# Performance work log

Measured on AMD Instinct MI355X. Metric: run time of the kernel, lower is better.

The kernel has to match this reference:

```python
import jax, jax.numpy as jnp
import numpy as np

N_QUERIES = 2000
N_DOCS = 128
FEATURE_DIM = 220
HIDDEN = 768
N_IDS = 65536


def setup_inputs() -> dict:
    key = jax.random.key(0)
    k1, k2, k3, k4, k5 = jax.random.split(key, 5)
    qid = jax.random.randint(k1, (N_IDS,), 0, N_QUERIES)
    did = jax.random.randint(k2, (N_IDS,), 0, N_DOCS)
    input_feature_id = jnp.stack([qid, did], axis=1).astype(jnp.int64)
    feature_table = jax.random.normal(k3, (N_QUERIES, N_DOCS, FEATURE_DIM), dtype=jnp.float32) * 10.0
    W = jax.random.normal(k4, (HIDDEN, FEATURE_DIM), dtype=jnp.float32) * (1.0 / np.sqrt(FEATURE_DIM))
    b = jax.random.normal(k5, (HIDDEN,), dtype=jnp.float32) * 0.01
    return {"input_feature_id": input_feature_id, "feature_table": feature_table, "W": W, "b": b}


def reference(input_feature_id, feature_table, W, b):
    # fused gather over (query, doc) ids: [N, FEATURE_DIM]
    feat = feature_table[input_feature_id[:, 0], input_feature_id[:, 1]]
    # log-sign transform: log(|x| + 1) * sign(x)
    feature_batch = jnp.log(jnp.abs(feat) + 1.0) * jnp.sign(feat)
    # Linear + ReLU (torch Linear: x @ W^T + b)
    output_embeds = jax.nn.relu(feature_batch @ W.T + b)
    return (output_embeds, feature_batch)
```

## Files before the change

kernel.cpp:

```cpp
#include <hip/hip_runtime.h>
#include <hip/hip_bf16.h>

#define M_TOTAL 65536
#define ND      128
#define FDIM    220
#define HID     768
#define G8      28
#define BSTRIDE 232

using bf16_t = __hip_bfloat16;
using bf16x8 = __attribute__((ext_vector_type(8))) short;
using f32x4  = __attribute__((ext_vector_type(4))) float;

struct __align__(16) bf16v8 { bf16_t v[8]; };

__device__ __forceinline__ float slog(float x) {
  return copysignf(log1pf(fabsf(x)), x);
}

__global__ __launch_bounds__(256) void gather_transform_kernel(
    const int2* __restrict__ ids, const float* __restrict__ table,
    float* __restrict__ fb)
{
  const int j   = blockIdx.x * 256 + threadIdx.x;
  const int row = j / G8;
  const int g   = j % G8;

  const int2 p = ids[row];
  const float* src = table + ((size_t)p.x * ND + p.y) * FDIM + g * 8;
  float*       dst = fb + (size_t)row * FDIM + g * 8;

  const float4 f0 = *(const float4*)src;
  float4 y0;
  y0.x = slog(f0.x); y0.y = slog(f0.y); y0.z = slog(f0.z); y0.w = slog(f0.w);
  *(float4*)dst = y0;

  if (g < 27) {
    const float4 f1 = *(const float4*)(src + 4);
    float4 y1;
    y1.x = slog(f1.x); y1.y = slog(f1.y); y1.z = slog(f1.z); y1.w = slog(f1.w);
    *(float4*)(dst + 4) = y1;
  }
}

__global__ __launch_bounds__(256, 2) void gemm_bias_relu_kernel(
    const float* __restrict__ A, const float* __restrict__ W,
    const float* __restrict__ bias, float* __restrict__ out)
{
  __shared__ bf16_t Bs[128 * BSTRIDE];

  const int tid = threadIdx.x;
  const int bn  = blockIdx.x;
  const int bm  = blockIdx.y;

#pragma unroll
  for (int it = 0; it < 14; ++it) {
    const int jj  = it * 256 + tid;
    const int row = jj / 28;
    const int g   = jj % 28;
    const float* src = W + (size_t)(bn * 128 + row) * FDIM + g * 8;
    const float4 f0 = *(const float4*)src;
    float4 f1;
    if (g < 27) {
      f1 = *(const float4*)(src + 4);
    } else {
      f1.x = 0.f; f1.y = 0.f; f1.z = 0.f; f1.w = 0.f;
    }
    bf16v8 h;
    h.v[0] = __float2bfloat16(f0.x); h.v[1] = __float2bfloat16(f0.y);
    h.v[2] = __float2bfloat16(f0.z); h.v[3] = __float2bfloat16(f0.w);
    h.v[4] = __float2bfloat16(f1.x); h.v[5] = __float2bfloat16(f1.y);
    h.v[6] = __float2bfloat16(f1.z); h.v[7] = __float2bfloat16(f1.w);
    *(bf16v8*)(Bs + row * BSTRIDE + g * 8) = h;
  }
  __syncthreads();

  const int wave = tid >> 6;
  const int lane = tid & 63;
  const int wm   = wave & 1;
  const int wn   = wave >> 1;
  const int l15  = lane & 15;
  const int q    = lane >> 4;

  f32x4 acc[4][4];
#pragma unroll
  for (int i = 0; i < 4; ++i)
#pragma unroll
    for (int j = 0; j < 4; ++j) acc[i][j] = (f32x4){0.f, 0.f, 0.f, 0.f};

  const float*  Abase  = A + (size_t)(bm * 128 + wm * 64 + l15) * FDIM + q * 8;
  const bf16_t* BsBase = Bs + (wn * 64 + l15) * BSTRIDE + q * 8;

#pragma unroll
  for (int kb = 0; kb < 7; ++kb) {
    bf16x8 af[4], bg[4];
#pragma unroll
    for (int mi = 0; mi < 4; ++mi) {
      const float* ap = Abase + (size_t)mi * 16 * FDIM + kb * 32;
      const float4 f0 = *(const float4*)ap;
      float4 f1;
      if (kb == 6 && q == 3) {
        f1.x = 0.f; f1.y = 0.f; f1.z = 0.f; f1.w = 0.f;
      } else {
        f1 = *(const float4*)(ap + 4);
      }
      bf16v8 h;
      h.v[0] = __float2bfloat16(f0.x); h.v[1] = __float2bfloat16(f0.y);
      h.v[2] = __float2bfloat16(f0.z); h.v[3] = __float2bfloat16(f0.w);
      h.v[4] = __float2bfloat16(f1.x); h.v[5] = __float2bfloat16(f1.y);
      h.v[6] = __float2bfloat16(f1.z); h.v[7] = __float2bfloat16(f1.w);
      af[mi] = *(const bf16x8*)&h;
    }
#pragma unroll
    for (int ni = 0; ni < 4; ++ni)
      bg[ni] = *(const bf16x8*)(BsBase + ni * 16 * BSTRIDE + kb * 32);
#pragma unroll
    for (int mi = 0; mi < 4; ++mi)
#pragma unroll
      for (int ni = 0; ni < 4; ++ni)
        acc[mi][ni] = __builtin_amdgcn_mfma_f32_16x16x32_bf16(
            af[mi], bg[ni], acc[mi][ni], 0, 0, 0);
  }

  const int col0 = bn * 128 + wn * 64 + l15;
  const int row0 = bm * 128 + wm * 64 + q * 4;
#pragma unroll
  for (int ni = 0; ni < 4; ++ni) {
    const int n    = col0 + ni * 16;
    const float bv = bias[n];
#pragma unroll
    for (int mi = 0; mi < 4; ++mi) {
#pragma unroll
      for (int r = 0; r < 4; ++r) {
        float v = acc[mi][ni][r] + bv;
        out[(size_t)(row0 + mi * 16 + r) * HID + n] = v > 0.f ? v : 0.f;
      }
    }
  }
}

extern "C" void kernel_launch(void* const* d_in, const int* in_sizes, int n_in,
                              void* d_out, int out_size, void* d_ws, size_t ws_size,
                              hipStream_t stream) {
  (void)in_sizes; (void)n_in; (void)out_size; (void)d_ws; (void)ws_size;

  const int2*  ids   = (const int2*)d_in[0];
  const float* table = (const float*)d_in[1];
  const float* W     = (const float*)d_in[2];
  const float* bias  = (const float*)d_in[3];

  float* out_embeds = (float*)d_out;
  float* fb_f32     = (float*)d_out + (size_t)M_TOTAL * HID;

  gather_transform_kernel<<<(M_TOTAL * G8) / 256, 256, 0, stream>>>(
      ids, table, fb_f32);

  dim3 grid(HID / 128, M_TOTAL / 128);
  gemm_bias_relu_kernel<<<grid, 256, 0, stream>>>(fb_f32, W, bias, out_embeds);
}
```

Measured before the change: 473.1 us.

## Fuse gather-transform into GEMM and pre-convert W to bf16

The gather plus log-sign transform now runs inside the GEMM kernel. Each block stages its 128 transformed rows as bf16 in shared memory, keeps the A fragments in registers, and loops over all six N tiles. W is converted once into a padded bf16 workspace by a small kernel and read directly from global memory. This removes the fp32 re-read of the feature batch and the repeated fp32-to-bf16 conversion of A, at the cost of fewer blocks (512), heavy register use for the A fragments, and B reads from global instead of LDS.

```diff
diff --git a/kernel.cpp b/kernel.cpp
--- a/kernel.cpp
+++ b/kernel.cpp
@@ -4,6 +4,7 @@
 #define M_TOTAL 65536
 #define ND      128
 #define FDIM    220
+#define KPAD    224
 #define HID     768
 #define G8      28
 #define BSTRIDE 232
@@ -18,60 +19,66 @@
   return copysignf(log1pf(fabsf(x)), x);
 }
 
-__global__ __launch_bounds__(256) void gather_transform_kernel(
-    const int2* __restrict__ ids, const float* __restrict__ table,
-    float* __restrict__ fb)
+__device__ __forceinline__ float4 slog4(float4 f) {
+  float4 y;
+  y.x = slog(f.x); y.y = slog(f.y); y.z = slog(f.z); y.w = slog(f.w);
+  return y;
+}
+
+__device__ __forceinline__ bf16v8 pack8(float4 a, float4 b) {
+  bf16v8 h;
+  h.v[0] = __float2bfloat16(a.x); h.v[1] = __float2bfloat16(a.y);
+  h.v[2] = __float2bfloat16(a.z); h.v[3] = __float2bfloat16(a.w);
+  h.v[4] = __float2bfloat16(b.x); h.v[5] = __float2bfloat16(b.y);
+  h.v[6] = __float2bfloat16(b.z); h.v[7] = __float2bfloat16(b.w);
+  return h;
+}
+
+__global__ __launch_bounds__(256) void convert_w_kernel(
+    const float* __restrict__ W, bf16_t* __restrict__ Wb)
 {
   const int j   = blockIdx.x * 256 + threadIdx.x;
   const int row = j / G8;
   const int g   = j % G8;
 
-  const int2 p = ids[row];
-  const float* src = table + ((size_t)p.x * ND + p.y) * FDIM + g * 8;
-  float*       dst = fb + (size_t)row * FDIM + g * 8;
-
+  const float* src = W + (size_t)row * FDIM + g * 8;
   const float4 f0 = *(const float4*)src;
-  float4 y0;
-  y0.x = slog(f0.x); y0.y = slog(f0.y); y0.z = slog(f0.z); y0.w = slog(f0.w);
-  *(float4*)dst = y0;
-
-  if (g < 27) {
-    const float4 f1 = *(const float4*)(src + 4);
-    float4 y1;
-    y1.x = slog(f1.x); y1.y = slog(f1.y); y1.z = slog(f1.z); y1.w = slog(f1.w);
-    *(float4*)(dst + 4) = y1;
-  }
+  float4 f1;
+  if (g < 27) f1 = *(const float4*)(src + 4);
+  else        { f1.x = 0.f; f1.y = 0.f; f1.z = 0.f; f1.w = 0.f; }
+  *(bf16v8*)(Wb + (size_t)row * KPAD + g * 8) = pack8(f0, f1);
 }
 
-__global__ __launch_bounds__(256, 2) void gemm_bias_relu_kernel(
-    const float* __restrict__ A, const float* __restrict__ W,
-    const float* __restrict__ bias, float* __restrict__ out)
+__global__ __launch_bounds__(256, 2) void fused_gather_gemm_kernel(
+    const int2* __restrict__ ids, const float* __restrict__ table,
+    const bf16_t* __restrict__ Wb, const float* __restrict__ bias,
+    float* __restrict__ out, float* __restrict__ fb)
 {
-  __shared__ bf16_t Bs[128 * BSTRIDE];
+  __shared__ bf16_t As[128 * BSTRIDE];
 
   const int tid = threadIdx.x;
-  const int bn  = blockIdx.x;
-  const int bm  = blockIdx.y;
+  const int bm  = blockIdx.x;
 
 #pragma unroll
   for (int it = 0; it < 14; ++it) {
-    const int jj  = it * 256 + tid;
-    const int row = jj / 28;
-    const int g   = jj % 28;
-    const float* src = W + (size_t)(bn * 128 + row) * FDIM + g * 8;
-    const float4 f0 = *(const float4*)src;
-    float4 f1;
+    const int jj   = it * 256 + tid;
+    const int row  = jj / G8;
+    const int g    = jj % G8;
+    const int grow = bm * 128 + row;
+    const int2 p   = ids[grow];
+    const float* src = table + ((size_t)p.x * ND + p.y) * FDIM + g * 8;
+    float*       dst = fb + (size_t)grow * FDIM + g * 8;
+
+    const float4 y0 = slog4(*(const float4*)src);
+    *(float4*)dst = y0;
+    float4 y1;
     if (g < 27) {
-      f1 = *(const float4*)(src + 4);
+      y1 = slog4(*(const float4*)(src + 4));
+      *(float4*)(dst + 4) = y1;
     } else {
-      f1.x = 0.f; f1.y = 0.f; f1.z = 0.f; f1.w = 0.f;
+      y1.x = 0.f; y1.y = 0.f; y1.z = 0.f; y1.w = 0.f;
     }
-    bf16v8 h;
-    h.v[0] = __float2bfloat16(f0.x); h.v[1] = __float2bfloat16(f0.y);
-    h.v[2] = __float2bfloat16(f0.z); h.v[3] = __float2bfloat16(f0.w);
-    h.v[4] = __float2bfloat16(f1.x); h.v[5] = __float2bfloat16(f1.y);
-    h.v[6] = __float2bfloat16(f1.z); h.v[7] = __float2bfloat16(f1.w);
-    *(bf16v8*)(Bs + row * BSTRIDE + g * 8) = h;
+    *(bf16v8*)(As + row * BSTRIDE + g * 8) = pack8(y0, y1);
   }
   __syncthreads();
 
@@ -82,58 +89,50 @@
   const int l15  = lane & 15;
   const int q    = lane >> 4;
 
-  f32x4 acc[4][4];
+  bf16x8 af[7][4];
 #pragma unroll
-  for (int i = 0; i < 4; ++i)
+  for (int kb = 0; kb < 7; ++kb)
 #pragma unroll
-    for (int j = 0; j < 4; ++j) acc[i][j] = (f32x4){0.f, 0.f, 0.f, 0.f};
+    for (int mi = 0; mi < 4; ++mi)
+      af[kb][mi] =
+          *(const bf16x8*)(As + (wm * 64 + mi * 16 + l15) * BSTRIDE + kb * 32 + q * 8);
 
-  const float*  Abase  = A + (size_t)(bm * 128 + wm * 64 + l15) * FDIM + q * 8;
-  const bf16_t* BsBase = Bs + (wn * 64 + l15) * BSTRIDE + q * 8;
+  for (int bn = 0; bn < 6; ++bn) {
+    f32x4 acc[4][4];
+#pragma unroll
+    for (int i = 0; i < 4; ++i)
+#pragma unroll
+      for (int j = 0; j < 4; ++j) acc[i][j] = (f32x4){0.f, 0.f, 0.f, 0.f};
+
+    const bf16_t* Wbase = Wb + (size_t)(bn * 128 + wn * 64 + l15) * KPAD + q * 8;
 
 #pragma unroll
-  for (int kb = 0; kb < 7; ++kb) {
-    bf16x8 af[4], bg[4];
-#pragma unroll
-    for (int mi = 0; mi < 4; ++mi) {
-      const float* ap = Abase + (size_t)mi * 16 * FDIM + kb * 32;
-      const float4 f0 = *(const float4*)ap;
-      float4 f1;
-      if (kb == 6 && q == 3) {
-        f1.x = 0.f; f1.y = 0.f; f1.z = 0.f; f1.w = 0.f;
-      } else {
-        f1 = *(const float4*)(ap + 4);
-      }
-      bf16v8 h;
-      h.v[0] = __float2bfloat16(f0.x); h.v[1] = __float2bfloat16(f0.y);
-      h.v[2] = __float2bfloat16(f0.z); h.v[3] = __float2bfloat16(f0.w);
-      h.v[4] = __float2bfloat16(f1.x); h.v[5] = __float2bfloat16(f1.y);
-      h.v[6] = __float2bfloat16(f1.z); h.v[7] = __float2bfloat16(f1.w);
-      af[mi] = *(const bf16x8*)&h;
-    }
-#pragma unroll
-    for (int ni = 0; ni < 4; ++ni)
-      bg[ni] = *(const bf16x8*)(BsBase + ni * 16 * BSTRIDE + kb * 32);
-#pragma unroll
-    for (int mi = 0; mi < 4; ++mi)
+    for (int kb = 0; kb < 7; ++kb) {
+      bf16x8 bg[4];
 #pragma unroll
       for (int ni = 0; ni < 4; ++ni)
-        acc[mi][ni] = __builtin_amdgcn_mfma_f32_16x16x32_bf16(
-            af[mi], bg[ni], acc[mi][ni], 0, 0, 0);
-  }
+        bg[ni] = *(const bf16x8*)(Wbase + (size_t)ni * 16 * KPAD + kb * 32);
+#pragma unroll
+      for (int mi = 0; mi < 4; ++mi)
+#pragma unroll
+        for (int ni = 0; ni < 4; ++ni)
+          acc[mi][ni] = __builtin_amdgcn_mfma_f32_16x16x32_bf16(
+              af[kb][mi], bg[ni], acc[mi][ni], 0, 0, 0);
+    }
 
-  const int col0 = bn * 128 + wn * 64 + l15;
-  const int row0 = bm * 128 + wm * 64 + q * 4;
+    const int col0 = bn * 128 + wn * 64 + l15;
+    const int row0 = bm * 128 + wm * 64 + q * 4;
 #pragma unroll
-  for (int ni = 0; ni < 4; ++ni) {
-    const int n    = col0 + ni * 16;
-    const float bv = bias[n];
+    for (int ni = 0; ni < 4; ++ni) {
+      const int n    = col0 + ni * 16;
+      const float bv = bias[n];
 #pragma unroll
-    for (int mi = 0; mi < 4; ++mi) {
+      for (int mi = 0; mi < 4; ++mi) {
 #pragma unroll
-      for (int r = 0; r < 4; ++r) {
-        float v = acc[mi][ni][r] + bv;
-        out[(size_t)(row0 + mi * 16 + r) * HID + n] = v > 0.f ? v : 0.f;
+        for (int r = 0; r < 4; ++r) {
+          float v = acc[mi][ni][r] + bv;
+          out[(size_t)(row0 + mi * 16 + r) * HID + n] = v > 0.f ? v : 0.f;
+        }
       }
     }
   }
@@ -142,7 +141,7 @@
 extern "C" void kernel_launch(void* const* d_in, const int* in_sizes, int n_in,
                               void* d_out, int out_size, void* d_ws, size_t ws_size,
                               hipStream_t stream) {
-  (void)in_sizes; (void)n_in; (void)out_size; (void)d_ws; (void)ws_size;
+  (void)in_sizes; (void)n_in; (void)out_size; (void)ws_size;
 
   const int2*  ids   = (const int2*)d_in[0];
   const float* table = (const float*)d_in[1];
@@ -152,9 +151,10 @@
   float* out_embeds = (float*)d_out;
   float* fb_f32     = (float*)d_out + (size_t)M_TOTAL * HID;
 
-  gather_transform_kernel<<<(M_TOTAL * G8) / 256, 256, 0, stream>>>(
-      ids, table, fb_f32);
+  bf16_t* Wb = (bf16_t*)d_ws;
 
-  dim3 grid(HID / 128, M_TOTAL / 128);
-  gemm_bias_relu_kernel<<<grid, 256, 0, stream>>>(fb_f32, W, bias, out_embeds);
+  convert_w_kernel<<<(HID * G8) / 256, 256, 0, stream>>>(W, Wb);
+
+  fused_gather_gemm_kernel<<<M_TOTAL / 128, 256, 0, stream>>>(
+      ids, table, Wb, bias, out_embeds, fb_f32);
 }
```

Result: faster. 423.1 us (-10.6%).
